# Performance work log

Hardware: AMD Instinct MI355X
Metric: run time of the kernel (lower is better)

## Reference

```python
import jax, jax.numpy as jnp
import numpy as np

N_GLOBAL = 100000
N_SUB = 50000
K = 20
IN_DIM = 256
OUT_DIM = 256
EPS = 1e-12  # F.normalize default eps


def setup_inputs() -> dict:
    key = jax.random.key(0)
    k1, k2, k3, k4, k5, k6, k7, k8 = jax.random.split(key, 8)
    X_sub = jax.random.normal(k1, (N_SUB, IN_DIM), dtype=jnp.float32)
    sub_nodes = jax.random.randint(k2, (N_SUB,), 0, N_GLOBAL, dtype=jnp.int64)
    graphsage_nbr_ids = jax.random.randint(k3, (N_GLOBAL, K), 0, N_GLOBAL, dtype=jnp.int64)
    # global->sub map with -1 sentinel for globals not in the subgraph
    global_to_sub = jax.random.randint(k4, (N_GLOBAL,), -1, N_SUB, dtype=jnp.int64)
    # Linear params (torch Linear: y = x @ W.T + b), Kaiming-uniform-ish scale
    s1 = 1.0 / np.sqrt(IN_DIM)
    W_nbr = jax.random.uniform(k5, (OUT_DIM, IN_DIM), jnp.float32, -s1, s1)
    b_nbr = jax.random.uniform(k6, (OUT_DIM,), jnp.float32, -s1, s1)
    s2 = 1.0 / np.sqrt(IN_DIM + OUT_DIM)
    W_final = jax.random.uniform(k7, (OUT_DIM, IN_DIM + OUT_DIM), jnp.float32, -s2, s2)
    b_final = jax.random.uniform(k8, (OUT_DIM,), jnp.float32, -s2, s2)
    return {
        "X_sub": X_sub,
        "sub_nodes": sub_nodes,
        "graphsage_nbr_ids": graphsage_nbr_ids,
        "global_to_sub": global_to_sub,
        "W_nbr": W_nbr,
        "b_nbr": b_nbr,
        "W_final": W_final,
        "b_final": b_final,
    }


def reference(X_sub, sub_nodes, graphsage_nbr_ids, global_to_sub,
              W_nbr, b_nbr, W_final, b_final):
    N_sub = X_sub.shape[0]
    node_expanded = graphsage_nbr_ids[sub_nodes]          # [N_sub, K] global ids
    sub_nbr_indices = global_to_sub[node_expanded]        # [N_sub, K] sub ids or -1
    row_idx = jnp.arange(N_sub)[:, None]                  # [N_sub, 1]
    sub_nbr_indices = jnp.where(sub_nbr_indices < 0, row_idx, sub_nbr_indices)
    nbr_mean = X_sub[sub_nbr_indices].mean(axis=1)        # [N_sub, in_dim]
    h_nbr = jax.nn.relu(nbr_mean @ W_nbr.T + b_nbr)       # [N_sub, out_dim]
    concat_vec = jnp.concatenate([X_sub, h_nbr], axis=1)  # [N_sub, in+out]
    out = jax.nn.relu(concat_vec @ W_final.T + b_final)   # [N_sub, out_dim]
    norm = jnp.linalg.norm(out, axis=1, keepdims=True)
    return out / jnp.maximum(norm, EPS)
```

## Files before the change

### kernel.cpp

```cpp
#include <hip/hip_runtime.h>
#include <hip/hip_bf16.h>

#define KNBR 20
typedef unsigned short u16;
typedef __attribute__((ext_vector_type(8))) short bf16x8;
typedef __attribute__((ext_vector_type(4))) float f32x4;

#define GLDS16(gsrc, ldst)                                                     \
    __builtin_amdgcn_global_load_lds(                                          \
        (const __attribute__((address_space(1))) unsigned int*)(const void*)(gsrc), \
        (__attribute__((address_space(3))) unsigned int*)(void*)(ldst), 16, 0, 0)

__device__ __forceinline__ bool idx_is64(const unsigned int* w) {
    return (w[1] | w[3] | w[5] | w[7] | w[9] | w[11] | w[13] | w[15]) == 0u;
}
__device__ __forceinline__ int idx_at(const int* p, bool is64, long long i) {
    return is64 ? p[2 * i] : p[i];
}
__device__ __forceinline__ u16 f2bf(float x) {
    union { __hip_bfloat16 b; u16 u; } cv;
    cv.b = __float2bfloat16(x);
    return cv.u;
}
__device__ __forceinline__ float blo2f(unsigned int w) {
    union { float f; unsigned int i; } c; c.i = w << 16; return c.f;
}
__device__ __forceinline__ float bhi2f(unsigned int w) {
    union { float f; unsigned int i; } c; c.i = w & 0xffff0000u; return c.f;
}

__global__ void __launch_bounds__(256) k_cast(
    const float* __restrict__ X, const float* __restrict__ Wn,
    const float* __restrict__ Wf, u16* __restrict__ Xb,
    u16* __restrict__ Wnb, u16* __restrict__ Wfb, int nx4)
{
    const int i = blockIdx.x * 256 + threadIdx.x;
    const float4* src; ushort4* dst; int j;
    if (i < nx4)                     { src = (const float4*)X;  dst = (ushort4*)Xb;  j = i; }
    else if (i < nx4 + 16384)        { src = (const float4*)Wn; dst = (ushort4*)Wnb; j = i - nx4; }
    else if (i < nx4 + 16384 + 32768){ src = (const float4*)Wf; dst = (ushort4*)Wfb; j = i - nx4 - 16384; }
    else return;
    const float4 v = src[j];
    ushort4 o;
    o.x = f2bf(v.x); o.y = f2bf(v.y); o.z = f2bf(v.z); o.w = f2bf(v.w);
    dst[j] = o;
}

__global__ void __launch_bounds__(512, 4) k_fused(
    const u16* __restrict__ Xb, const int* __restrict__ sub_nodes,
    const int* __restrict__ nbr, const int* __restrict__ g2s,
    const u16* __restrict__ Wnb, const float* __restrict__ bn,
    const u16* __restrict__ Wfb, const float* __restrict__ bfin,
    float* __restrict__ Out, int M)
{
    __shared__ u16 mh[64 * 256];
    __shared__ u16 Bs[2][256 * 32];
    __shared__ u16 Xs[2][64 * 32];
    __shared__ __align__(16) float sums[64][4];

    const int t    = threadIdx.x;
    const int lane = t & 63;
    const int w    = t >> 6;
    const int wm   = w >> 2;
    const int wn   = w & 3;
    const int l15  = lane & 15;
    const int lk8  = (lane >> 4) << 3;
    const int rsub = (lane >> 4) << 2;
    const int r7   = l15 & 7;
    const int r3   = l15 & 3;
    const int sRow = lane >> 2;
    const int sSlot= lane & 3;
    const int m0   = blockIdx.x * 64;

#define STAGE_B(buf, Bp, KT, tt) do {                                          \
    _Pragma("unroll")                                                          \
    for (int rp_ = 0; rp_ < 2; ++rp_) {                                        \
        const int rr_ = rp_ * 128 + w * 16 + sRow;                             \
        const int cc_ = sSlot ^ (rr_ & 3);                                     \
        GLDS16(Bp + (size_t)rr_ * KT + (tt) * 32 + cc_ * 8,                    \
               &Bs[buf][rp_ * 4096 + w * 512]);                                \
    } } while (0)

#define STAGE_X(buf, tt) do {                                                  \
    if (w < 4) {                                                               \
        const int rl_ = w * 16 + sRow;                                         \
        int rg_ = m0 + rl_; rg_ = (rg_ < M) ? rg_ : (M - 1);                   \
        const int cc_ = sSlot ^ (rl_ & 3);                                     \
        GLDS16(Xb + (size_t)rg_ * 256 + (tt) * 32 + cc_ * 8, &Xs[buf][w * 512]); \
    } } while (0)

    STAGE_B(0, Wnb, 256, 0);

    {
        const bool is64 = idx_is64((const unsigned int*)nbr);
        const int half = lane >> 5;
        const int l31  = lane & 31;
        const int sb   = half << 5;
        #pragma unroll 1
        for (int j = 0; j < 4; ++j) {
            const int rl  = w * 8 + j * 2 + half;
            const int row = m0 + rl;
            const int rowc = (row < M) ? row : (M - 1);
            const int g = idx_at(sub_nodes, is64, rowc);
            int s_my = rowc;
            if (l31 < KNBR) {
                int nid = idx_at(nbr, is64, (long long)g * KNBR + l31);
                int s   = idx_at(g2s, is64, nid);
                s_my = (s < 0) ? rowc : s;
            }
            uint4 v[KNBR];
            #pragma unroll
            for (int k = 0; k < KNBR; ++k) {
                const int sk = __shfl(s_my, sb + k, 64);
                v[k] = *(const uint4*)(Xb + (size_t)sk * 256 + l31 * 8);
            }
            float a0=0.f,a1=0.f,a2=0.f,a3=0.f,a4=0.f,a5=0.f,a6=0.f,a7=0.f;
            #pragma unroll
            for (int k = 0; k < KNBR; ++k) {
                a0 += blo2f(v[k].x); a1 += bhi2f(v[k].x);
                a2 += blo2f(v[k].y); a3 += bhi2f(v[k].y);
                a4 += blo2f(v[k].z); a5 += bhi2f(v[k].z);
                a6 += blo2f(v[k].w); a7 += bhi2f(v[k].w);
            }
            const float inv = 1.0f / (float)KNBR;
            uint4 o;
            o.x = (unsigned)f2bf(a0*inv) | ((unsigned)f2bf(a1*inv) << 16);
            o.y = (unsigned)f2bf(a2*inv) | ((unsigned)f2bf(a3*inv) << 16);
            o.z = (unsigned)f2bf(a4*inv) | ((unsigned)f2bf(a5*inv) << 16);
            o.w = (unsigned)f2bf(a6*inv) | ((unsigned)f2bf(a7*inv) << 16);
            *(uint4*)&mh[rl * 256 + ((l31 ^ (rl & 7)) << 3)] = o;
        }
    }
    __syncthreads();

    f32x4 acc[2][4];
    #pragma unroll
    for (int i = 0; i < 2; ++i)
        #pragma unroll
        for (int j = 0; j < 4; ++j)
            acc[i][j] = (f32x4)(0.f);

    #pragma unroll
    for (int tt = 0; tt < 8; ++tt) {
        const int cur = tt & 1;
        if (tt < 7) STAGE_B(cur ^ 1, Wnb, 256, tt + 1);
        bf16x8 af[2], bfr[4];
        #pragma unroll
        for (int fm = 0; fm < 2; ++fm)
            af[fm] = *(const bf16x8*)&mh[(wm*32 + fm*16 + l15) * 256 +
                                         (((tt*4 + (lk8 >> 3)) ^ r7) << 3)];
        #pragma unroll
        for (int fn = 0; fn < 4; ++fn)
            bfr[fn] = *(const bf16x8*)&Bs[cur][(wn*64 + fn*16 + l15) * 32 +
                                              (((lk8 >> 3) ^ r3) << 3)];
        #pragma unroll
        for (int fm = 0; fm < 2; ++fm)
            #pragma unroll
            for (int fn = 0; fn < 4; ++fn)
                acc[fm][fn] = __builtin_amdgcn_mfma_f32_16x16x32_bf16(
                    af[fm], bfr[fn], acc[fm][fn], 0, 0, 0);
        __syncthreads();
    }

    STAGE_B(0, Wfb, 512, 0);
    STAGE_X(0, 0);

    #pragma unroll
    for (int fn = 0; fn < 4; ++fn) {
        const int col = wn * 64 + fn * 16 + l15;
        const float bv = bn[col];
        #pragma unroll
        for (int fm = 0; fm < 2; ++fm)
            #pragma unroll
            for (int r = 0; r < 4; ++r) {
                const int row = wm * 32 + fm * 16 + rsub + r;
                const float v = fmaxf(acc[fm][fn][r] + bv, 0.f);
                mh[row * 256 + ((((col >> 3) ^ (row & 7))) << 3) + (col & 7)] = f2bf(v);
            }
    }
    __syncthreads();

    #pragma unroll
    for (int i = 0; i < 2; ++i)
        #pragma unroll
        for (int j = 0; j < 4; ++j)
            acc[i][j] = (f32x4)(0.f);

    #pragma unroll
    for (int tt = 0; tt < 16; ++tt) {
        const int cur = tt & 1;
        if (tt < 15) {
            STAGE_B(cur ^ 1, Wfb, 512, tt + 1);
            if (tt + 1 < 8) STAGE_X(cur ^ 1, tt + 1);
        }
        bf16x8 af[2], bfr[4];
        if (tt < 8) {
            #pragma unroll
            for (int fm = 0; fm < 2; ++fm)
                af[fm] = *(const bf16x8*)&Xs[cur][(wm*32 + fm*16 + l15) * 32 +
                                                  (((lk8 >> 3) ^ r3) << 3)];
        } else {
            #pragma unroll
            for (int fm = 0; fm < 2; ++fm)
                af[fm] = *(const bf16x8*)&mh[(wm*32 + fm*16 + l15) * 256 +
                                             ((((tt-8)*4 + (lk8 >> 3)) ^ r7) << 3)];
        }
        #pragma unroll
        for (int fn = 0; fn < 4; ++fn)
            bfr[fn] = *(const bf16x8*)&Bs[cur][(wn*64 + fn*16 + l15) * 32 +
                                              (((lk8 >> 3) ^ r3) << 3)];
        #pragma unroll
        for (int fm = 0; fm < 2; ++fm)
            #pragma unroll
            for (int fn = 0; fn < 4; ++fn)
                acc[fm][fn] = __builtin_amdgcn_mfma_f32_16x16x32_bf16(
                    af[fm], bfr[fn], acc[fm][fn], 0, 0, 0);
        __syncthreads();
    }

    float part[2][4];
    #pragma unroll
    for (int fm = 0; fm < 2; ++fm)
        #pragma unroll
        for (int r = 0; r < 4; ++r)
            part[fm][r] = 0.f;
    #pragma unroll
    for (int fn = 0; fn < 4; ++fn) {
        const float bv = bfin[wn * 64 + fn * 16 + l15];
        #pragma unroll
        for (int fm = 0; fm < 2; ++fm)
            #pragma unroll
            for (int r = 0; r < 4; ++r) {
                const float v = fmaxf(acc[fm][fn][r] + bv, 0.f);
                acc[fm][fn][r] = v;
                part[fm][r] += v * v;
            }
    }
    #pragma unroll
    for (int fm = 0; fm < 2; ++fm)
        #pragma unroll
        for (int r = 0; r < 4; ++r) {
            float s = part[fm][r];
            s += __shfl_xor(s, 1, 64);
            s += __shfl_xor(s, 2, 64);
            s += __shfl_xor(s, 4, 64);
            s += __shfl_xor(s, 8, 64);
            part[fm][r] = s;
        }
    if (l15 == 0) {
        #pragma unroll
        for (int fm = 0; fm < 2; ++fm)
            #pragma unroll
            for (int r = 0; r < 4; ++r)
                sums[wm * 32 + fm * 16 + rsub + r][wn] = part[fm][r];
    }
    __syncthreads();
    #pragma unroll
    for (int fm = 0; fm < 2; ++fm)
        #pragma unroll
        for (int r = 0; r < 4; ++r) {
            const int lrow = wm * 32 + fm * 16 + rsub + r;
            const f32x4 sv = *(const f32x4*)&sums[lrow][0];
            const float tot = sv.x + sv.y + sv.z + sv.w;
            const float scale = 1.f / fmaxf(sqrtf(tot), 1e-12f);
            const int row = m0 + lrow;
            if (row < M) {
                #pragma unroll
                for (int fn = 0; fn < 4; ++fn)
                    Out[(size_t)row * 256 + wn * 64 + fn * 16 + l15] =
                        acc[fm][fn][r] * scale;
            }
        }
#undef STAGE_B
#undef STAGE_X
}

extern "C" void kernel_launch(void* const* d_in, const int* in_sizes, int n_in,
                              void* d_out, int out_size, void* d_ws, size_t ws_size,
                              hipStream_t stream)
{
    const float* X         = (const float*)d_in[0];
    const int*   sub_nodes = (const int*)d_in[1];
    const int*   nbr       = (const int*)d_in[2];
    const int*   g2s       = (const int*)d_in[3];
    const float* Wn        = (const float*)d_in[4];
    const float* bn        = (const float*)d_in[5];
    const float* Wf        = (const float*)d_in[6];
    const float* bfin      = (const float*)d_in[7];
    float*       out       = (float*)d_out;

    const int M = out_size / 256;

    u16* Xb  = (u16*)d_ws;
    u16* Wnb = Xb  + (size_t)M * 256;
    u16* Wfb = Wnb + 65536;

    const int nx4 = M * 64;
    const int castTotal = nx4 + 16384 + 32768;
    k_cast<<<(castTotal + 255) / 256, 256, 0, stream>>>(X, Wn, Wf, Xb, Wnb, Wfb, nx4);

    const int fBlocks = (M + 63) / 64;
    k_fused<<<fBlocks, 512, 0, stream>>>(Xb, sub_nodes, nbr, g2s,
                                         Wnb, bn, Wfb, bfin, out, M);
}
```

Baseline: 126.1 us.

## Single-buffer weight and X LDS tiles to raise occupancy

Drops the double-buffered LDS staging of the weight tiles and X tiles in favour of single buffers. Each k-step now becomes compute, barrier, load the next tile, barrier, instead of prefetching during compute. The LDS footprint shrinks, which allows more resident blocks per CU, and the launch-bounds hint is raised from 4 to 6 to match. In exchange, global-to-LDS latency is no longer overlapped with MFMA work, each step gains an extra barrier, and the tighter occupancy hint may cap VGPRs low enough to cause spills.

```diff
diff --git a/kernel.cpp b/kernel.cpp
--- a/kernel.cpp
+++ b/kernel.cpp
@@ -46,7 +46,7 @@
     dst[j] = o;
 }
 
-__global__ void __launch_bounds__(512, 4) k_fused(
+__global__ void __launch_bounds__(512, 6) k_fused(
     const u16* __restrict__ Xb, const int* __restrict__ sub_nodes,
     const int* __restrict__ nbr, const int* __restrict__ g2s,
     const u16* __restrict__ Wnb, const float* __restrict__ bn,
@@ -54,8 +54,8 @@
     float* __restrict__ Out, int M)
 {
     __shared__ u16 mh[64 * 256];
-    __shared__ u16 Bs[2][256 * 32];
-    __shared__ u16 Xs[2][64 * 32];
+    __shared__ u16 Bs[256 * 32];
+    __shared__ u16 Xs[64 * 32];
     __shared__ __align__(16) float sums[64][4];
 
     const int t    = threadIdx.x;
@@ -72,24 +72,24 @@
     const int sSlot= lane & 3;
     const int m0   = blockIdx.x * 64;
 
-#define STAGE_B(buf, Bp, KT, tt) do {                                          \
+#define STAGE_B(Bp, KT, tt) do {                                               \
     _Pragma("unroll")                                                          \
     for (int rp_ = 0; rp_ < 2; ++rp_) {                                        \
         const int rr_ = rp_ * 128 + w * 16 + sRow;                             \
         const int cc_ = sSlot ^ (rr_ & 3);                                     \
         GLDS16(Bp + (size_t)rr_ * KT + (tt) * 32 + cc_ * 8,                    \
-               &Bs[buf][rp_ * 4096 + w * 512]);                                \
+               &Bs[rp_ * 4096 + w * 512]);                                     \
     } } while (0)
 
-#define STAGE_X(buf, tt) do {                                                  \
+#define STAGE_X(tt) do {                                                       \
     if (w < 4) {                                                               \
         const int rl_ = w * 16 + sRow;                                         \
         int rg_ = m0 + rl_; rg_ = (rg_ < M) ? rg_ : (M - 1);                   \
         const int cc_ = sSlot ^ (rl_ & 3);                                     \
-        GLDS16(Xb + (size_t)rg_ * 256 + (tt) * 32 + cc_ * 8, &Xs[buf][w * 512]); \
+        GLDS16(Xb + (size_t)rg_ * 256 + (tt) * 32 + cc_ * 8, &Xs[w * 512]);    \
     } } while (0)
 
-    STAGE_B(0, Wnb, 256, 0);
+    STAGE_B(Wnb, 256, 0);
 
     {
         const bool is64 = idx_is64((const unsigned int*)nbr);
@@ -142,8 +142,6 @@
 
     #pragma unroll
     for (int tt = 0; tt < 8; ++tt) {
-        const int cur = tt & 1;
-        if (tt < 7) STAGE_B(cur ^ 1, Wnb, 256, tt + 1);
         bf16x8 af[2], bfr[4];
         #pragma unroll
         for (int fm = 0; fm < 2; ++fm)
@@ -151,8 +149,8 @@
                                          (((tt*4 + (lk8 >> 3)) ^ r7) << 3)];
         #pragma unroll
         for (int fn = 0; fn < 4; ++fn)
-            bfr[fn] = *(const bf16x8*)&Bs[cur][(wn*64 + fn*16 + l15) * 32 +
-                                              (((lk8 >> 3) ^ r3) << 3)];
+            bfr[fn] = *(const bf16x8*)&Bs[(wn*64 + fn*16 + l15) * 32 +
+                                          (((lk8 >> 3) ^ r3) << 3)];
         #pragma unroll
         for (int fm = 0; fm < 2; ++fm)
             #pragma unroll
@@ -160,10 +158,10 @@
                 acc[fm][fn] = __builtin_amdgcn_mfma_f32_16x16x32_bf16(
                     af[fm], bfr[fn], acc[fm][fn], 0, 0, 0);
         __syncthreads();
-    }
-
-    STAGE_B(0, Wfb, 512, 0);
-    STAGE_X(0, 0);
+        if (tt < 7) STAGE_B(Wnb, 256, tt + 1);
+        else        { STAGE_B(Wfb, 512, 0); STAGE_X(0); }
+        __syncthreads();
+    }
 
     #pragma unroll
     for (int fn = 0; fn < 4; ++fn) {
@@ -188,17 +186,12 @@
 
     #pragma unroll
     for (int tt = 0; tt < 16; ++tt) {
-        const int cur = tt & 1;
-        if (tt < 15) {
-            STAGE_B(cur ^ 1, Wfb, 512, tt + 1);
-            if (tt + 1 < 8) STAGE_X(cur ^ 1, tt + 1);
-        }
         bf16x8 af[2], bfr[4];
         if (tt < 8) {
             #pragma unroll
             for (int fm = 0; fm < 2; ++fm)
-                af[fm] = *(const bf16x8*)&Xs[cur][(wm*32 + fm*16 + l15) * 32 +
-                                                  (((lk8 >> 3) ^ r3) << 3)];
+                af[fm] = *(const bf16x8*)&Xs[(wm*32 + fm*16 + l15) * 32 +
+                                             (((lk8 >> 3) ^ r3) << 3)];
         } else {
             #pragma unroll
             for (int fm = 0; fm < 2; ++fm)
@@ -207,14 +200,19 @@
         }
         #pragma unroll
         for (int fn = 0; fn < 4; ++fn)
-            bfr[fn] = *(const bf16x8*)&Bs[cur][(wn*64 + fn*16 + l15) * 32 +
-                                              (((lk8 >> 3) ^ r3) << 3)];
+            bfr[fn] = *(const bf16x8*)&Bs[(wn*64 + fn*16 + l15) * 32 +
+                                          (((lk8 >> 3) ^ r3) << 3)];
         #pragma unroll
         for (int fm = 0; fm < 2; ++fm)
             #pragma unroll
             for (int fn = 0; fn < 4; ++fn)
                 acc[fm][fn] = __builtin_amdgcn_mfma_f32_16x16x32_bf16(
                     af[fm], bfr[fn], acc[fm][fn], 0, 0, 0);
+        __syncthreads();
+        if (tt < 15) {
+            STAGE_B(Wfb, 512, tt + 1);
+            if (tt + 1 < 8) STAGE_X(tt + 1);
+        }
         __syncthreads();
     }
 
```

Measured after the change: 167.2 us. 1.33x slower.
